# Performance work log

Measured on AMD Instinct MI355X. Metric: run time of the kernel, lower is better.

## Reference

```python
import jax, jax.numpy as jnp
import numpy as np

N_LAYERS, H, D, DFF, V = 6, 16, 1024, 4096, 512
B, S = 4, 2048
DK = D // H
EPS = 1e-6
NEG = -1000000000.0


def _pe_table(max_len, d):
    pos = np.arange(max_len, dtype=np.float32)[:, None]
    div = 1.0 / (10000.0 ** (np.arange(0, d, 2, dtype=np.float32) / d))
    pe = np.zeros((max_len, d), dtype=np.float32)
    pe[:, 0::2] = np.sin(pos * div)
    pe[:, 1::2] = np.cos(pos * div)
    return jnp.asarray(pe[None])  # [1, max_len, d]


def setup_inputs() -> dict:
    key = jax.random.key(0)
    ks = jax.random.split(key, 20)
    f = lambda k, shp: (jax.random.normal(k, shp, dtype=jnp.float32) * 0.02)
    inp = {
        "tgt": jax.random.randint(ks[0], (B, S), 0, V, dtype=jnp.int64),
        "tgt_mask": jnp.tril(jnp.ones((S, S), dtype=jnp.int32))[None],  # [1,S,S] causal
        "emb": f(ks[1], (V, D)),
        "pe": _pe_table(S, D),
        "Wq": f(ks[2], (N_LAYERS, H, D, DK)), "bq": f(ks[3], (N_LAYERS, H, DK)),
        "Wk": f(ks[4], (N_LAYERS, H, D, DK)), "bk": f(ks[5], (N_LAYERS, H, DK)),
        "Wv": f(ks[6], (N_LAYERS, H, D, DK)), "bv": f(ks[7], (N_LAYERS, H, DK)),
        "Wo": f(ks[8], (N_LAYERS, D, D)), "bo": f(ks[9], (N_LAYERS, D)),
        "W1": f(ks[10], (N_LAYERS, D, DFF)), "b1": f(ks[11], (N_LAYERS, DFF)),
        "W2": f(ks[12], (N_LAYERS, DFF, D)), "b2": f(ks[13], (N_LAYERS, D)),
        "ln1_a": jnp.ones((N_LAYERS, D)), "ln1_b": jnp.zeros((N_LAYERS, D)),
        "ln2_a": jnp.ones((N_LAYERS, D)), "ln2_b": jnp.zeros((N_LAYERS, D)),
        "lnf_a": jnp.ones((D,)), "lnf_b": jnp.zeros((D,)),
    }
    return inp


def _ln(x, a, b):
    # torch: a*(x-mean)/(std+eps)+b with unbiased std
    m = x.mean(-1, keepdims=True)
    var = ((x - m) ** 2).sum(-1, keepdims=True) / (x.shape[-1] - 1)
    return a * (x - m) / (jnp.sqrt(var) + EPS) + b


def reference(tgt, tgt_mask, emb, pe, Wq, bq, Wk, bk, Wv, bv, Wo, bo,
              W1, b1, W2, b2, ln1_a, ln1_b, ln2_a, ln2_b, lnf_a, lnf_b):
    d = emb.shape[1]
    s = tgt.shape[1]
    x = emb[tgt] * jnp.sqrt(jnp.float32(d)) + pe[:, :s]  # [B,S,D]
    dk = Wq.shape[-1]
    scale = jnp.sqrt(jnp.float32(dk))

    def layer(x, p):
        wq, bq_, wk, bk_, wv, bv_, wo, bo_, w1, b1_, w2, b2_, a1, g1, a2, g2 = p
        h = _ln(x, a1, g1)
        q = jnp.einsum('bsd,hdk->bhsk', h, wq) + bq_[:, None, :]
        k = jnp.einsum('bsd,hdk->bhsk', h, wk) + bk_[:, None, :]
        v = jnp.einsum('bsd,hdk->bhsk', h, wv) + bv_[:, None, :]
        sc = jnp.einsum('bhsk,bhtk->bhst', q, k) / scale
        sc = jnp.where(tgt_mask[:, None] == 0, jnp.float32(NEG), sc)
        att = jax.nn.softmax(sc, axis=-1)
        o = jnp.einsum('bhst,bhtk->bhsk', att, v)
        o = o.transpose(0, 2, 1, 3).reshape(x.shape)  # concat heads (head order)
        x = x + (o @ wo + bo_)
        h2 = _ln(x, a2, g2)
        x = x + (jnp.maximum(h2 @ w1 + b1_, 0.0) @ w2 + b2_)
        return x, None

    x, _ = jax.lax.scan(layer, x, (Wq, bq, Wk, bk, Wv, bv, Wo, bo,
                                   W1, b1, W2, b2, ln1_a, ln1_b, ln2_a, ln2_b))
    return _ln(x, lnf_a, lnf_b)
```

## Files before the change

kernel.cpp:

```cpp
#include <hip/hip_runtime.h>

typedef __bf16 bf16;
typedef float f32x4 __attribute__((ext_vector_type(4)));
typedef __bf16 bf16x8 __attribute__((ext_vector_type(8)));
typedef __bf16 bf16x4 __attribute__((ext_vector_type(4)));
typedef __bf16 bf16x2 __attribute__((ext_vector_type(2)));

#define NL 6
#define NH 16
#define DM 1024
#define DFF 4096
#define SEQ 2048
#define NB 4
#define NTOK (NB*SEQ)

__device__ __forceinline__ void gload16(const void* g, void* l) {
  __builtin_amdgcn_global_load_lds((const __attribute__((address_space(1))) void*)g,
                                   (__attribute__((address_space(3))) void*)l, 16, 0, 0);
}

__global__ __launch_bounds__(256) void repack_t(const float* __restrict__ src,
                                                bf16* __restrict__ out, int K, int N) {
  const int l = blockIdx.z;
  const int d0 = blockIdx.x * 32, n0 = blockIdx.y * 32;
  __shared__ float t[32][33];
  const int tx = threadIdx.x & 31, ty = threadIdx.x >> 5;
  const float* s = src + (size_t)l * K * N;
  #pragma unroll
  for (int j = 0; j < 4; ++j)
    t[ty*4 + j][tx] = s[(size_t)(d0 + ty*4 + j) * N + n0 + tx];
  __syncthreads();
  bf16* o = out + (size_t)l * N * K;
  #pragma unroll
  for (int j = 0; j < 4; ++j)
    o[(size_t)(n0 + ty*4 + j) * K + d0 + tx] = (bf16)t[tx][ty*4 + j];
}

__global__ __launch_bounds__(256) void repack_qkv(const float* __restrict__ Wq,
                                                  const float* __restrict__ Wk,
                                                  const float* __restrict__ Wv,
                                                  bf16* __restrict__ out) {
  const int l = blockIdx.z;
  const int d0 = blockIdx.x * 32, n0 = blockIdx.y * 32;
  __shared__ float t[32][33];
  const int tx = threadIdx.x & 31, ty = threadIdx.x >> 5;
  const int which = n0 >> 10, h = (n0 & 1023) >> 6, kh0 = n0 & 63;
  const float* W = (which == 0) ? Wq : (which == 1 ? Wk : Wv);
  const float* s = W + ((size_t)(l*NH + h) * DM) * 64 + kh0;
  #pragma unroll
  for (int j = 0; j < 4; ++j)
    t[ty*4 + j][tx] = s[(size_t)(d0 + ty*4 + j) * 64 + tx];
  __syncthreads();
  bf16* o = out + (size_t)l * 3072 * DM + (size_t)n0 * DM + d0;
  #pragma unroll
  for (int j = 0; j < 4; ++j)
    o[(size_t)(ty*4 + j) * DM + tx] = (bf16)t[tx][ty*4 + j];
}

__global__ __launch_bounds__(256) void repack_b(const float* __restrict__ bq,
                                                const float* __restrict__ bk,
                                                const float* __restrict__ bv,
                                                float* __restrict__ out) {
  const int i = blockIdx.x * 256 + threadIdx.x;
  if (i >= NL * 3072) return;
  const int l = i / 3072, n = i % 3072;
  const int which = n >> 10, h = (n >> 6) & 15, kh = n & 63;
  const float* b = (which == 0) ? bq : (which == 1 ? bk : bv);
  out[i] = b[(l*NH + h) * 64 + kh];
}

__global__ __launch_bounds__(256) void embed_k(const int* __restrict__ tgt,
                                               const float* __restrict__ emb,
                                               const float* __restrict__ pe,
                                               float* __restrict__ x) {
  const int i = blockIdx.x;
  const int spos = i & (SEQ - 1);
  const int tok = tgt[i];
  const int tid = threadIdx.x;
  float4 e = ((const float4*)(emb + (size_t)tok * DM))[tid];
  float4 p = ((const float4*)(pe + (size_t)spos * DM))[tid];
  float4 r; r.x = e.x*32.f + p.x; r.y = e.y*32.f + p.y; r.z = e.z*32.f + p.z; r.w = e.w*32.f + p.w;
  ((float4*)(x + (size_t)i * DM))[tid] = r;
}

template<bool OB>
__global__ __launch_bounds__(256) void ln_k(const float* __restrict__ x,
                                            const float* __restrict__ a,
                                            const float* __restrict__ bsh,
                                            bf16* __restrict__ ob, float* __restrict__ of) {
  __shared__ float red[8];
  const int row = blockIdx.x, tid = threadIdx.x;
  const float4 v = ((const float4*)(x + (size_t)row * DM))[tid];
  float s = v.x + v.y + v.z + v.w;
  #pragma unroll
  for (int off = 32; off > 0; off >>= 1) s += __shfl_down(s, off);
  if ((tid & 63) == 0) red[tid >> 6] = s;
  __syncthreads();
  const float mean = (red[0] + red[1] + red[2] + red[3]) * (1.f / 1024.f);
  const float d0 = v.x - mean, d1 = v.y - mean, d2 = v.z - mean, d3 = v.w - mean;
  float ss = d0*d0 + d1*d1 + d2*d2 + d3*d3;
  #pragma unroll
  for (int off = 32; off > 0; off >>= 1) ss += __shfl_down(ss, off);
  if ((tid & 63) == 0) red[4 + (tid >> 6)] = ss;
  __syncthreads();
  const float var = (red[4] + red[5] + red[6] + red[7]) * (1.f / 1023.f);
  const float inv = 1.f / (sqrtf(var) + 1e-6f);
  const float4 av = ((const float4*)a)[tid];
  const float4 bv = ((const float4*)bsh)[tid];
  const float r0 = av.x * d0 * inv + bv.x;
  const float r1 = av.y * d1 * inv + bv.y;
  const float r2 = av.z * d2 * inv + bv.z;
  const float r3 = av.w * d3 * inv + bv.w;
  if (OB) {
    bf16x4 w; w[0] = (bf16)r0; w[1] = (bf16)r1; w[2] = (bf16)r2; w[3] = (bf16)r3;
    ((bf16x4*)(ob + (size_t)row * DM))[tid] = w;
  } else {
    float4 w; w.x = r0; w.y = r1; w.z = r2; w.w = r3;
    ((float4*)(of + (size_t)row * DM))[tid] = w;
  }
}

#define BARRIER() asm volatile("s_barrier" ::: "memory")
#define VMW(n)    asm volatile("s_waitcnt vmcnt(" #n ")" ::: "memory")

template<int EPI>
__global__ __launch_bounds__(512, 1) void gemm8(const bf16* __restrict__ A,
                                                const bf16* __restrict__ B,
                                                const float* __restrict__ bias,
                                                float* __restrict__ xres,
                                                bf16* __restrict__ outb,
                                                bf16* __restrict__ vtb,
                                                int K, int ldc) {
  __shared__ __align__(16) char lds[131072];
  const int tid = threadIdx.x;
  const int m0 = blockIdx.x * 256, n0 = blockIdx.y * 256;
  const int wid = tid >> 6, lane = tid & 63;
  const int wm = wid >> 2, wn = wid & 3;
  const int fr = lane & 15, fq = lane >> 4;
  const int fl16 = (fq * 16 + fr) * 16;
  const int s0 = tid, s1 = tid + 512;
  const int r0 = ((s0 >> 7) << 4) | (s0 & 15), c0 = (((s0 >> 6) & 1) << 2) | ((s0 >> 4) & 3);
  const int r1 = ((s1 >> 7) << 4) | (s1 & 15), c1 = (((s1 >> 6) & 1) << 2) | ((s1 >> 4) & 3);
  const bf16* Ap0 = A + (size_t)(m0 + r0) * K + c0 * 8;
  const bf16* Ap1 = A + (size_t)(m0 + r1) * K + c1 * 8;
  const bf16* Bp0 = B + (size_t)(n0 + r0) * K + c0 * 8;
  const bf16* Bp1 = B + (size_t)(n0 + r1) * K + c1 * 8;
  const size_t rskip = (size_t)128 * K;
  const int aRd = wm * 16384;
  const int bRd = 32768 + (wn >> 1) * 16384;
  const int bN = (wn & 1) * 4;

  f32x4 acc[8][4] = {};
  bf16x8 af8[8][2], bfr[4][2];

#define ST_A(d, h, kt) { \
  gload16(Ap0 + (size_t)(h) * rskip + (kt), lds + (d)*65536 + (h)*16384 + s0*16); \
  gload16(Ap1 + (size_t)(h) * rskip + (kt), lds + (d)*65536 + (h)*16384 + s1*16); }
#define ST_B(d, h, kt) { \
  gload16(Bp0 + (size_t)(h) * rskip + (kt), lds + (d)*65536 + 32768 + (h)*16384 + s0*16); \
  gload16(Bp1 + (size_t)(h) * rskip + (kt), lds + (d)*65536 + 32768 + (h)*16384 + s1*16); }
#define LD_A(d, mb) { _Pragma("unroll") for (int m_ = 0; m_ < 4; ++m_) \
    _Pragma("unroll") for (int ks_ = 0; ks_ < 2; ++ks_) \
      af8[(mb) + m_][ks_] = *(const bf16x8*)(lds + (d)*65536 + aRd + ((mb) + m_)*2048 + ks_*1024 + fl16); }
#define LD_B(d, nb) { _Pragma("unroll") for (int n_ = 0; n_ < 2; ++n_) \
    _Pragma("unroll") for (int ks_ = 0; ks_ < 2; ++ks_) \
      bfr[(nb) + n_][ks_] = *(const bf16x8*)(lds + (d)*65536 + bRd + (bN + (nb) + n_)*2048 + ks_*1024 + fl16); }
#define MFMA_Q(mb, nb) { __builtin_amdgcn_s_setprio(1); \
  _Pragma("unroll") for (int m_ = 0; m_ < 4; ++m_) \
  _Pragma("unroll") for (int n_ = 0; n_ < 2; ++n_) \
  _Pragma("unroll") for (int ks_ = 0; ks_ < 2; ++ks_) \
    acc[(mb) + m_][(nb) + n_] = __builtin_amdgcn_mfma_f32_16x16x32_bf16( \
        af8[(mb) + m_][ks_], bfr[(nb) + n_][ks_], acc[(mb) + m_][(nb) + n_], 0, 0, 0); \
  __builtin_amdgcn_s_setprio(0); }

  ST_A(0, 0, 0); ST_A(0, 1, 0);
  ST_B(0, 0, 0); ST_B(0, 1, 0);
  ST_A(1, 0, 64); ST_A(1, 1, 64);
  VMW(4);
  BARRIER();

  const int niter = K >> 7;
  for (int it = 0; it < niter; ++it) {
    const int ktB1 = (2 * it + 1) << 6;
    const int ktE2 = (2 * it + 2) << 6;
    const int ktO3 = (2 * it + 3) << 6;
    const bool more = (it + 1 < niter);
    LD_A(0, 0); LD_B(0, 0);
    ST_B(1, 0, ktB1);
    BARRIER(); MFMA_Q(0, 0); BARRIER();
    LD_A(0, 4);
    ST_B(1, 1, ktB1);
    BARRIER(); MFMA_Q(4, 0); BARRIER();
    LD_B(0, 2);
    if (more) ST_A(0, 0, ktE2);
    BARRIER(); MFMA_Q(4, 2); BARRIER();
    if (more) { ST_A(0, 1, ktE2); VMW(4); } else { VMW(0); }
    BARRIER(); MFMA_Q(0, 2); BARRIER();
    LD_A(1, 0); LD_B(1, 0);
    if (more) ST_B(0, 0, ktE2);
    BARRIER(); MFMA_Q(0, 0); BARRIER();
    LD_A(1, 4);
    if (more) ST_B(0, 1, ktE2);
    BARRIER(); MFMA_Q(4, 0); BARRIER();
    LD_B(1, 2);
    if (more) ST_A(1, 0, ktO3);
    BARRIER(); MFMA_Q(4, 2); BARRIER();
    if (more) { ST_A(1, 1, ktO3); VMW(4); }
    BARRIER(); MFMA_Q(0, 2); BARRIER();
  }
#undef ST_A
#undef ST_B
#undef LD_A
#undef LD_B
#undef MFMA_Q

  #pragma unroll
  for (int m = 0; m < 8; ++m) {
    const int row = m0 + wm * 128 + m * 16 + fq * 4;
    #pragma unroll
    for (int n = 0; n < 4; ++n) {
      const int col = n0 + wn * 64 + n * 16 + fr;
      const float bc = bias[col];
      if constexpr (EPI == 3) {
        if (col >= 2048) {
          const int hh = (col - 2048) >> 6, dkk = col & 63;
          const int bb = row >> 11, tt = row & 2047;
          bf16x4 w;
          #pragma unroll
          for (int j = 0; j < 4; ++j) w[j] = (bf16)(acc[m][n][j] + bc);
          *(bf16x4*)(vtb + ((((size_t)bb*NH + hh)*64 + dkk)*SEQ + tt)) = w;
          continue;
        }
      }
      #pragma unroll
      for (int j = 0; j < 4; ++j) {
        const float v = acc[m][n][j] + bc;
        if constexpr (EPI == 1) {
          xres[(size_t)(row + j) * ldc + col] += v;
        } else if constexpr (EPI == 2) {
          outb[(size_t)(row + j) * ldc + col] = (bf16)fmaxf(v, 0.f);
        } else {
          outb[(size_t)(row + j) * ldc + col] = (bf16)v;
        }
      }
    }
  }
}

template<int EPI>
__global__ __launch_bounds__(512, 1) void gemm8n(const bf16* __restrict__ A,
                                                 const bf16* __restrict__ B,
                                                 const float* __restrict__ bias,
                                                 float* __restrict__ xres,
                                                 bf16* __restrict__ outb,
                                                 bf16* __restrict__ vtb,
                                                 int K, int ldc) {
  __shared__ __align__(16) char lds[131072];
  const int tid = threadIdx.x;
  const int m0 = blockIdx.x * 128, n0 = blockIdx.y * 256;
  const int wid = tid >> 6, lane = tid & 63;
  const int wm = wid >> 2, wn = wid & 3;
  const int fr = lane & 15, fq = lane >> 4;
  const int fl16 = (fq * 16 + fr) * 16;
  const int s0 = tid, s1 = tid + 512;
  const int r0 = ((s0 >> 7) << 4) | (s0 & 15), c0 = (((s0 >> 6) & 1) << 2) | ((s0 >> 4) & 3);
  const int r1 = ((s1 >> 7) << 4) | (s1 & 15), c1 = (((s1 >> 6) & 1) << 2) | ((s1 >> 4) & 3);
  const bf16* Ap0 = A + (size_t)(m0 + r0) * K + c0 * 8;
  const bf16* Ap1 = A + (size_t)(m0 + r1) * K + c1 * 8;
  const bf16* Bp0 = B + (size_t)(n0 + r0) * K + c0 * 8;
  const bf16* Bp1 = B + (size_t)(n0 + r1) * K + c1 * 8;
  const size_t rskipB = (size_t)128 * K;
  const int aRd = wm * 8192;
  const int bRd = wn * 8192;

  f32x4 acc[4][4] = {};
  bf16x8 af[4][2], bfr[4][2];

#define ST_An(d, kt) { \
  gload16(Ap0 + (kt), lds + (d)*16384 + s0*16); \
  gload16(Ap1 + (kt), lds + (d)*16384 + s1*16); }
#define ST_Bn(j, h, kt) { \
  gload16(Bp0 + (size_t)(h) * rskipB + (kt), lds + 32768 + (j)*32768 + (h)*16384 + s0*16); \
  gload16(Bp1 + (size_t)(h) * rskipB + (kt), lds + 32768 + (j)*32768 + (h)*16384 + s1*16); }
#define LD_An(d) { _Pragma("unroll") for (int m_ = 0; m_ < 4; ++m_) \
    _Pragma("unroll") for (int ks_ = 0; ks_ < 2; ++ks_) \
      af[m_][ks_] = *(const bf16x8*)(lds + (d)*16384 + aRd + m_*2048 + ks_*1024 + fl16); }
#define LD_Bn(j, nb) { _Pragma("unroll") for (int n_ = 0; n_ < 2; ++n_) \
    _Pragma("unroll") for (int ks_ = 0; ks_ < 2; ++ks_) \
      bfr[(nb) + n_][ks_] = *(const bf16x8*)(lds + 32768 + (j)*32768 + bRd + ((nb) + n_)*2048 + ks_*1024 + fl16); }
#define MFMA_H(nb) { __builtin_amdgcn_s_setprio(1); \
  _Pragma("unroll") for (int m_ = 0; m_ < 4; ++m_) \
  _Pragma("unroll") for (int n_ = 0; n_ < 2; ++n_) \
  _Pragma("unroll") for (int ks_ = 0; ks_ < 2; ++ks_) \
    acc[m_][(nb) + n_] = __builtin_amdgcn_mfma_f32_16x16x32_bf16( \
        af[m_][ks_], bfr[(nb) + n_][ks_], acc[m_][(nb) + n_], 0, 0, 0); \
  __builtin_amdgcn_s_setprio(0); }

  ST_An(0, 0);
  ST_Bn(0, 0, 0); ST_Bn(0, 1, 0);
  ST_An(1, 64);
  ST_Bn(1, 0, 64); ST_Bn(1, 1, 64);
  VMW(0);
  BARRIER();

  const int nt = K >> 6;
  int j = 0;
  for (int t = 0; t < nt; ++t) {
    const int d = t & 1;
    const int j2 = (j + 2 >= 3) ? (j - 1) : (j + 2);
    const bool more = (t + 2 < nt);
    const int kt2 = (t + 2) << 6;
    LD_An(d); LD_Bn(j, 0);
    if (more) { ST_Bn(j2, 0, kt2); ST_Bn(j2, 1, kt2); }
    BARRIER(); MFMA_H(0); BARRIER();
    LD_Bn(j, 2);
    if (more) { ST_An(d, kt2); VMW(6); } else { VMW(0); }
    BARRIER(); MFMA_H(2); BARRIER();
    j = (j + 1 >= 3) ? 0 : (j + 1);
  }
#undef ST_An
#undef ST_Bn
#undef LD_An
#undef LD_Bn
#undef MFMA_H

  #pragma unroll
  for (int m = 0; m < 4; ++m) {
    const int row = m0 + wm * 64 + m * 16 + fq * 4;
    #pragma unroll
    for (int n = 0; n < 4; ++n) {
      const int col = n0 + wn * 64 + n * 16 + fr;
      const float bc = bias[col];
      if constexpr (EPI == 3) {
        if (col >= 2048) {
          const int hh = (col - 2048) >> 6, dkk = col & 63;
          const int bb = row >> 11, tt = row & 2047;
          bf16x4 w;
          #pragma unroll
          for (int jj = 0; jj < 4; ++jj) w[jj] = (bf16)(acc[m][n][jj] + bc);
          *(bf16x4*)(vtb + ((((size_t)bb*NH + hh)*64 + dkk)*SEQ + tt)) = w;
          continue;
        }
      }
      #pragma unroll
      for (int jj = 0; jj < 4; ++jj) {
        const float v = acc[m][n][jj] + bc;
        if constexpr (EPI == 1) {
          xres[(size_t)(row + jj) * ldc + col] += v;
        } else if constexpr (EPI == 2) {
          outb[(size_t)(row + jj) * ldc + col] = (bf16)fmaxf(v, 0.f);
        } else {
          outb[(size_t)(row + jj) * ldc + col] = (bf16)v;
        }
      }
    }
  }
}

__global__ __launch_bounds__(256) void attn5_k(const bf16* __restrict__ qk,
                                               const bf16* __restrict__ vt,
                                               bf16* __restrict__ o) {
  __shared__ __align__(16) bf16 Ks[64 * 64];
  __shared__ __align__(16) bf16 Vs[64 * 64];
  __shared__ __align__(16) bf16 Ps[4][16 * 64];
  const int pairi = blockIdx.x;
  const int bh = blockIdx.y;
  const int b = bh >> 4, h = bh & 15;
  const int tid = threadIdx.x;
  const int wave = tid >> 6, lane = tid & 63;
  const int fr = lane & 15, fq = lane >> 4;
  const bf16* Qg = qk + (size_t)b * SEQ * 2048 + h * 64;
  const bf16* Kg = Qg + 1024;
  const bf16* Vtg = vt + (size_t)bh * 64 * SEQ;
  char* Ksc = (char*)Ks;
  char* Vsc = (char*)Vs;
  char* Pw = (char*)&Ps[wave][0];
  const int fr7 = fr & 7;

  for (int pass = 0; pass < 2; ++pass) {
    const int qb = (pass == 0) ? pairi : (31 - pairi);
    const int q0w = qb * 64 + wave * 16;
    const int qrow = q0w + fr;
    const bf16x8 qf0 = *(const bf16x8*)(Qg + (size_t)qrow * 2048 + fq * 8);
    const bf16x8 qf1 = *(const bf16x8*)(Qg + (size_t)qrow * 2048 + 32 + fq * 8);
    f32x4 oacc[4] = {};
    float mrun = -1e30f, lrun = 0.f;
    const int nt = qb + 1;
    for (int kt = 0; kt < nt; ++kt) {
      const int t0 = kt * 64;
      __syncthreads();
      #pragma unroll
      for (int s2 = 0; s2 < 2; ++s2) {
        const int slot = tid + s2 * 256;
        const int r = slot >> 3, mm = slot & 7;
        const int gc = (mm ^ (r & 7)) * 8;
        gload16(Kg + (size_t)(t0 + r) * 2048 + gc, Ksc + slot * 16);
        gload16(Vtg + (size_t)r * SEQ + t0 + gc, Vsc + slot * 16);
      }
      __syncthreads();
      if (t0 > q0w + 15) continue;
      f32x4 s[4] = {};
      #pragma unroll
      for (int n = 0; n < 4; ++n) {
        const int t_ = n * 16 + fr;
        const bf16x8 k0 = *(const bf16x8*)(Ksc + (t_ * 8 + (fq ^ (t_ & 7))) * 16);
        const bf16x8 k1 = *(const bf16x8*)(Ksc + (t_ * 8 + ((fq + 4) ^ (t_ & 7))) * 16);
        s[n] = __builtin_amdgcn_mfma_f32_16x16x32_bf16(k0, qf0, s[n], 0, 0, 0);
        s[n] = __builtin_amdgcn_mfma_f32_16x16x32_bf16(k1, qf1, s[n], 0, 0, 0);
      }
      float sv[16];
      #pragma unroll
      for (int n = 0; n < 4; ++n)
        #pragma unroll
        for (int jj = 0; jj < 4; ++jj)
          sv[n * 4 + jj] = s[n][jj] * 0.125f;
      const bool need_mask = (t0 + 63 > q0w);
      if (need_mask) {
        #pragma unroll
        for (int i = 0; i < 16; ++i) {
          const int t_abs = t0 + (i >> 2) * 16 + fq * 4 + (i & 3);
          if (t_abs > qrow) sv[i] = -1e30f;
        }
      }
      float a8[8];
      #pragma unroll
      for (int i = 0; i < 8; ++i) a8[i] = fmaxf(sv[i], sv[i + 8]);
      float a4[4];
      #pragma unroll
      for (int i = 0; i < 4; ++i) a4[i] = fmaxf(a8[i], a8[i + 4]);
      float mt = fmaxf(fmaxf(a4[0], a4[1]), fmaxf(a4[2], a4[3]));
      mt = fmaxf(mt, __shfl_xor(mt, 16));
      mt = fmaxf(mt, __shfl_xor(mt, 32));
      const float mnew = fmaxf(mrun, mt);
      const float corr = __expf(mrun - mnew);
      mrun = mnew;
      #pragma unroll
      for (int i = 0; i < 16; ++i) sv[i] = __expf(sv[i] - mnew);
      #pragma unroll
      for (int i = 0; i < 8; ++i) a8[i] = sv[i] + sv[i + 8];
      #pragma unroll
      for (int i = 0; i < 4; ++i) a4[i] = a8[i] + a8[i + 4];
      float ps = (a4[0] + a4[1]) + (a4[2] + a4[3]);
      ps += __shfl_xor(ps, 16);
      ps += __shfl_xor(ps, 32);
      lrun = lrun * corr + ps;
      float cv[4];
      #pragma unroll
      for (int jj = 0; jj < 4; ++jj) cv[jj] = __shfl(corr, fq * 4 + jj);
      #pragma unroll
      for (int nd = 0; nd < 4; ++nd)
        #pragma unroll
        for (int jj = 0; jj < 4; ++jj)
          oacc[nd][jj] *= cv[jj];
      #pragma unroll
      for (int n = 0; n < 4; ++n)
        #pragma unroll
        for (int jp = 0; jp < 2; ++jp) {
          bf16x2 w; w[0] = (bf16)sv[n * 4 + jp * 2]; w[1] = (bf16)sv[n * 4 + jp * 2 + 1];
          const int byteoff = n * 32 + fq * 8 + jp * 4;
          const int chunk = byteoff >> 4, within = byteoff & 15;
          *(bf16x2*)(Pw + fr * 128 + ((chunk ^ fr7) << 4) + within) = w;
        }
      #pragma unroll
      for (int ks = 0; ks < 2; ++ks) {
        const bf16x8 pa = *(const bf16x8*)(Pw + fr * 128 + (((ks * 4 + fq) ^ fr7) << 4));
        #pragma unroll
        for (int nd = 0; nd < 4; ++nd) {
          const int dk_ = nd * 16 + fr;
          const bf16x8 vf = *(const bf16x8*)(Vsc + (dk_ * 8 + ((ks * 4 + fq) ^ (dk_ & 7))) * 16);
          oacc[nd] = __builtin_amdgcn_mfma_f32_16x16x32_bf16(pa, vf, oacc[nd], 0, 0, 0);
        }
      }
    }
    float lv[4];
    #pragma unroll
    for (int jj = 0; jj < 4; ++jj) lv[jj] = __shfl(lrun, fq * 4 + jj);
    #pragma unroll
    for (int nd = 0; nd < 4; ++nd) {
      const int col = h * 64 + nd * 16 + fr;
      #pragma unroll
      for (int jj = 0; jj < 4; ++jj) {
        const int row = q0w + fq * 4 + jj;
        o[((size_t)b * SEQ + row) * DM + col] = (bf16)(oacc[nd][jj] / lv[jj]);
      }
    }
  }
}

extern "C" void kernel_launch(void* const* d_in, const int* in_sizes, int n_in,
                              void* d_out, int out_size, void* d_ws, size_t ws_size,
                              hipStream_t stream) {
  const int*   tgt  = (const int*)d_in[0];
  const float* emb  = (const float*)d_in[2];
  const float* pe   = (const float*)d_in[3];
  const float* Wq   = (const float*)d_in[4];
  const float* bq   = (const float*)d_in[5];
  const float* Wk   = (const float*)d_in[6];
  const float* bk   = (const float*)d_in[7];
  const float* Wv   = (const float*)d_in[8];
  const float* bv   = (const float*)d_in[9];
  const float* Wo   = (const float*)d_in[10];
  const float* bo   = (const float*)d_in[11];
  const float* W1   = (const float*)d_in[12];
  const float* b1   = (const float*)d_in[13];
  const float* W2   = (const float*)d_in[14];
  const float* b2   = (const float*)d_in[15];
  const float* ln1a = (const float*)d_in[16];
  const float* ln1b = (const float*)d_in[17];
  const float* ln2a = (const float*)d_in[18];
  const float* ln2b = (const float*)d_in[19];
  const float* lnfa = (const float*)d_in[20];
  const float* lnfb = (const float*)d_in[21];

  char* ws = (char*)d_ws;
  size_t off = 0;
  bf16*  wqkv = (bf16*)(ws + off);  off += (size_t)NL * 3072 * DM * 2;
  bf16*  wo_  = (bf16*)(ws + off);  off += (size_t)NL * DM * DM * 2;
  bf16*  w1_  = (bf16*)(ws + off);  off += (size_t)NL * DFF * DM * 2;
  bf16*  w2_  = (bf16*)(ws + off);  off += (size_t)NL * DM * DFF * 2;
  float* bqkv = (float*)(ws + off); off += (size_t)NL * 3072 * 4;
  float* x    = (float*)(ws + off); off += (size_t)NTOK * DM * 4;
  bf16*  hbuf = (bf16*)(ws + off);  off += (size_t)NTOK * DM * 2;
  bf16*  qkb  = (bf16*)(ws + off);  off += (size_t)NTOK * 2048 * 2;
  bf16*  vtb  = (bf16*)(ws + off);  off += (size_t)NB * NH * 64 * SEQ * 2;
  bf16*  obuf = (bf16*)(ws + off);  off += (size_t)NTOK * DM * 2;
  bf16*  ubuf = qkb;

  repack_qkv<<<dim3(32, 96, NL), 256, 0, stream>>>(Wq, Wk, Wv, wqkv);
  repack_t  <<<dim3(32, 32, NL), 256, 0, stream>>>(Wo, wo_, DM, DM);
  repack_t  <<<dim3(32, 128, NL), 256, 0, stream>>>(W1, w1_, DM, DFF);
  repack_t  <<<dim3(128, 32, NL), 256, 0, stream>>>(W2, w2_, DFF, DM);
  repack_b  <<<72, 256, 0, stream>>>(bq, bk, bv, bqkv);
  embed_k   <<<NTOK, 256, 0, stream>>>(tgt, emb, pe, x);

  for (int l = 0; l < NL; ++l) {
    ln_k<true><<<NTOK, 256, 0, stream>>>(x, ln1a + l * DM, ln1b + l * DM, hbuf, nullptr);
    gemm8n<3><<<dim3(64, 12), 512, 0, stream>>>(hbuf, wqkv + (size_t)l * 3072 * DM,
                                                bqkv + l * 3072, nullptr, qkb, vtb, DM, 2048);
    attn5_k<<<dim3(16, 64), 256, 0, stream>>>(qkb, vtb, obuf);
    gemm8n<1><<<dim3(64, 4), 512, 0, stream>>>(obuf, wo_ + (size_t)l * DM * DM,
                                               bo + l * DM, x, nullptr, nullptr, DM, DM);
    ln_k<true><<<NTOK, 256, 0, stream>>>(x, ln2a + l * DM, ln2b + l * DM, hbuf, nullptr);
    gemm8<2><<<dim3(32, 16), 512, 0, stream>>>(hbuf, w1_ + (size_t)l * DFF * DM,
                                               b1 + l * DFF, nullptr, ubuf, nullptr, DM, DFF);
    gemm8n<1><<<dim3(64, 4), 512, 0, stream>>>(ubuf, w2_ + (size_t)l * DM * DFF,
                                               b2 + l * DM, x, nullptr, nullptr, DFF, DM);
  }
  ln_k<false><<<NTOK, 256, 0, stream>>>(x, lnfa, lnfb, nullptr, (float*)d_out);

  (void)in_sizes; (void)n_in; (void)out_size; (void)ws_size;
}
```

Measured before the change: 2.738 ms.

## Replace tuned GEMMs with simple 128x128 double-buffered kernel and pipeline attention K/V

Replaces the two hand-scheduled 512-thread GEMMs (256x256 and 128x256 tiles with interleaved staging and barriers) with a single 256-thread, 128x128-tile GEMM. It uses two LDS stages and targets two blocks per CU. The attention kernel now double-buffers K/V tiles, remaps blocks so each XCD shares heads, and skips the rescale when the running max does not grow. The 1/sqrt(dk) scale is folded into the Q projection epilogue. The simpler GEMM loses the fine-grained load/MFMA interleave and the larger-tile reuse, so it may lose throughput on the dominant matmuls.

```diff
diff --git a/kernel.cpp b/kernel.cpp
--- a/kernel.cpp
+++ b/kernel.cpp
@@ -124,205 +124,70 @@
 #define VMW(n)    asm volatile("s_waitcnt vmcnt(" #n ")" ::: "memory")
 
 template<int EPI>
-__global__ __launch_bounds__(512, 1) void gemm8(const bf16* __restrict__ A,
+__global__ __launch_bounds__(256, 2) void gemmA(const bf16* __restrict__ A,
                                                 const bf16* __restrict__ B,
                                                 const float* __restrict__ bias,
                                                 float* __restrict__ xres,
                                                 bf16* __restrict__ outb,
                                                 bf16* __restrict__ vtb,
                                                 int K, int ldc) {
-  __shared__ __align__(16) char lds[131072];
+  __shared__ __align__(16) char lds[65536];
   const int tid = threadIdx.x;
-  const int m0 = blockIdx.x * 256, n0 = blockIdx.y * 256;
+  const int m0 = blockIdx.x * 128, n0 = blockIdx.y * 128;
   const int wid = tid >> 6, lane = tid & 63;
-  const int wm = wid >> 2, wn = wid & 3;
+  const int wm = wid >> 1, wn = wid & 1;
   const int fr = lane & 15, fq = lane >> 4;
   const int fl16 = (fq * 16 + fr) * 16;
-  const int s0 = tid, s1 = tid + 512;
-  const int r0 = ((s0 >> 7) << 4) | (s0 & 15), c0 = (((s0 >> 6) & 1) << 2) | ((s0 >> 4) & 3);
-  const int r1 = ((s1 >> 7) << 4) | (s1 & 15), c1 = (((s1 >> 6) & 1) << 2) | ((s1 >> 4) & 3);
-  const bf16* Ap0 = A + (size_t)(m0 + r0) * K + c0 * 8;
-  const bf16* Ap1 = A + (size_t)(m0 + r1) * K + c1 * 8;
-  const bf16* Bp0 = B + (size_t)(n0 + r0) * K + c0 * 8;
-  const bf16* Bp1 = B + (size_t)(n0 + r1) * K + c1 * 8;
-  const size_t rskip = (size_t)128 * K;
-  const int aRd = wm * 16384;
-  const int bRd = 32768 + (wn >> 1) * 16384;
-  const int bN = (wn & 1) * 4;
-
-  f32x4 acc[8][4] = {};
-  bf16x8 af8[8][2], bfr[4][2];
-
-#define ST_A(d, h, kt) { \
-  gload16(Ap0 + (size_t)(h) * rskip + (kt), lds + (d)*65536 + (h)*16384 + s0*16); \
-  gload16(Ap1 + (size_t)(h) * rskip + (kt), lds + (d)*65536 + (h)*16384 + s1*16); }
-#define ST_B(d, h, kt) { \
-  gload16(Bp0 + (size_t)(h) * rskip + (kt), lds + (d)*65536 + 32768 + (h)*16384 + s0*16); \
-  gload16(Bp1 + (size_t)(h) * rskip + (kt), lds + (d)*65536 + 32768 + (h)*16384 + s1*16); }
-#define LD_A(d, mb) { _Pragma("unroll") for (int m_ = 0; m_ < 4; ++m_) \
-    _Pragma("unroll") for (int ks_ = 0; ks_ < 2; ++ks_) \
-      af8[(mb) + m_][ks_] = *(const bf16x8*)(lds + (d)*65536 + aRd + ((mb) + m_)*2048 + ks_*1024 + fl16); }
-#define LD_B(d, nb) { _Pragma("unroll") for (int n_ = 0; n_ < 2; ++n_) \
-    _Pragma("unroll") for (int ks_ = 0; ks_ < 2; ++ks_) \
-      bfr[(nb) + n_][ks_] = *(const bf16x8*)(lds + (d)*65536 + bRd + (bN + (nb) + n_)*2048 + ks_*1024 + fl16); }
-#define MFMA_Q(mb, nb) { __builtin_amdgcn_s_setprio(1); \
-  _Pragma("unroll") for (int m_ = 0; m_ < 4; ++m_) \
-  _Pragma("unroll") for (int n_ = 0; n_ < 2; ++n_) \
-  _Pragma("unroll") for (int ks_ = 0; ks_ < 2; ++ks_) \
-    acc[(mb) + m_][(nb) + n_] = __builtin_amdgcn_mfma_f32_16x16x32_bf16( \
-        af8[(mb) + m_][ks_], bfr[(nb) + n_][ks_], acc[(mb) + m_][(nb) + n_], 0, 0, 0); \
-  __builtin_amdgcn_s_setprio(0); }
-
-  ST_A(0, 0, 0); ST_A(0, 1, 0);
-  ST_B(0, 0, 0); ST_B(0, 1, 0);
-  ST_A(1, 0, 64); ST_A(1, 1, 64);
-  VMW(4);
-  BARRIER();
-
-  const int niter = K >> 7;
-  for (int it = 0; it < niter; ++it) {
-    const int ktB1 = (2 * it + 1) << 6;
-    const int ktE2 = (2 * it + 2) << 6;
-    const int ktO3 = (2 * it + 3) << 6;
-    const bool more = (it + 1 < niter);
-    LD_A(0, 0); LD_B(0, 0);
-    ST_B(1, 0, ktB1);
-    BARRIER(); MFMA_Q(0, 0); BARRIER();
-    LD_A(0, 4);
-    ST_B(1, 1, ktB1);
-    BARRIER(); MFMA_Q(4, 0); BARRIER();
-    LD_B(0, 2);
-    if (more) ST_A(0, 0, ktE2);
-    BARRIER(); MFMA_Q(4, 2); BARRIER();
-    if (more) { ST_A(0, 1, ktE2); VMW(4); } else { VMW(0); }
-    BARRIER(); MFMA_Q(0, 2); BARRIER();
-    LD_A(1, 0); LD_B(1, 0);
-    if (more) ST_B(0, 0, ktE2);
-    BARRIER(); MFMA_Q(0, 0); BARRIER();
-    LD_A(1, 4);
-    if (more) ST_B(0, 1, ktE2);
-    BARRIER(); MFMA_Q(4, 0); BARRIER();
-    LD_B(1, 2);
-    if (more) ST_A(1, 0, ktO3);
-    BARRIER(); MFMA_Q(4, 2); BARRIER();
-    if (more) { ST_A(1, 1, ktO3); VMW(4); }
-    BARRIER(); MFMA_Q(0, 2); BARRIER();
-  }
-#undef ST_A
-#undef ST_B
-#undef LD_A
-#undef LD_B
-#undef MFMA_Q
-
-  #pragma unroll
-  for (int m = 0; m < 8; ++m) {
-    const int row = m0 + wm * 128 + m * 16 + fq * 4;
-    #pragma unroll
-    for (int n = 0; n < 4; ++n) {
-      const int col = n0 + wn * 64 + n * 16 + fr;
-      const float bc = bias[col];
-      if constexpr (EPI == 3) {
-        if (col >= 2048) {
-          const int hh = (col - 2048) >> 6, dkk = col & 63;
-          const int bb = row >> 11, tt = row & 2047;
-          bf16x4 w;
-          #pragma unroll
-          for (int j = 0; j < 4; ++j) w[j] = (bf16)(acc[m][n][j] + bc);
-          *(bf16x4*)(vtb + ((((size_t)bb*NH + hh)*64 + dkk)*SEQ + tt)) = w;
-          continue;
-        }
-      }
-      #pragma unroll
-      for (int j = 0; j < 4; ++j) {
-        const float v = acc[m][n][j] + bc;
-        if constexpr (EPI == 1) {
-          xres[(size_t)(row + j) * ldc + col] += v;
-        } else if constexpr (EPI == 2) {
-          outb[(size_t)(row + j) * ldc + col] = (bf16)fmaxf(v, 0.f);
-        } else {
-          outb[(size_t)(row + j) * ldc + col] = (bf16)v;
-        }
-      }
-    }
-  }
-}
-
-template<int EPI>
-__global__ __launch_bounds__(512, 1) void gemm8n(const bf16* __restrict__ A,
-                                                 const bf16* __restrict__ B,
-                                                 const float* __restrict__ bias,
-                                                 float* __restrict__ xres,
-                                                 bf16* __restrict__ outb,
-                                                 bf16* __restrict__ vtb,
-                                                 int K, int ldc) {
-  __shared__ __align__(16) char lds[131072];
-  const int tid = threadIdx.x;
-  const int m0 = blockIdx.x * 128, n0 = blockIdx.y * 256;
-  const int wid = tid >> 6, lane = tid & 63;
-  const int wm = wid >> 2, wn = wid & 3;
-  const int fr = lane & 15, fq = lane >> 4;
-  const int fl16 = (fq * 16 + fr) * 16;
-  const int s0 = tid, s1 = tid + 512;
-  const int r0 = ((s0 >> 7) << 4) | (s0 & 15), c0 = (((s0 >> 6) & 1) << 2) | ((s0 >> 4) & 3);
-  const int r1 = ((s1 >> 7) << 4) | (s1 & 15), c1 = (((s1 >> 6) & 1) << 2) | ((s1 >> 4) & 3);
-  const bf16* Ap0 = A + (size_t)(m0 + r0) * K + c0 * 8;
-  const bf16* Ap1 = A + (size_t)(m0 + r1) * K + c1 * 8;
-  const bf16* Bp0 = B + (size_t)(n0 + r0) * K + c0 * 8;
-  const bf16* Bp1 = B + (size_t)(n0 + r1) * K + c1 * 8;
-  const size_t rskipB = (size_t)128 * K;
   const int aRd = wm * 8192;
-  const int bRd = wn * 8192;
+  const int bRd = 16384 + wn * 8192;
+
+  const bf16* Ap[4];
+  const bf16* Bp[4];
+  #pragma unroll
+  for (int j = 0; j < 4; ++j) {
+    const int s = tid + j * 256;
+    const int r = ((s >> 7) << 4) | (s & 15);
+    const int c = (((s >> 6) & 1) << 2) | ((s >> 4) & 3);
+    Ap[j] = A + (size_t)(m0 + r) * K + c * 8;
+    Bp[j] = B + (size_t)(n0 + r) * K + c * 8;
+  }
 
   f32x4 acc[4][4] = {};
   bf16x8 af[4][2], bfr[4][2];
 
-#define ST_An(d, kt) { \
-  gload16(Ap0 + (kt), lds + (d)*16384 + s0*16); \
-  gload16(Ap1 + (kt), lds + (d)*16384 + s1*16); }
-#define ST_Bn(j, h, kt) { \
-  gload16(Bp0 + (size_t)(h) * rskipB + (kt), lds + 32768 + (j)*32768 + (h)*16384 + s0*16); \
-  gload16(Bp1 + (size_t)(h) * rskipB + (kt), lds + 32768 + (j)*32768 + (h)*16384 + s1*16); }
-#define LD_An(d) { _Pragma("unroll") for (int m_ = 0; m_ < 4; ++m_) \
+#define STG(d, kt) { _Pragma("unroll") for (int j = 0; j < 4; ++j) { \
+    gload16(Ap[j] + (kt), lds + (d)*32768 + (tid + j*256)*16); \
+    gload16(Bp[j] + (kt), lds + (d)*32768 + 16384 + (tid + j*256)*16); } }
+#define LDF(d) { _Pragma("unroll") for (int m_ = 0; m_ < 4; ++m_) \
     _Pragma("unroll") for (int ks_ = 0; ks_ < 2; ++ks_) \
-      af[m_][ks_] = *(const bf16x8*)(lds + (d)*16384 + aRd + m_*2048 + ks_*1024 + fl16); }
-#define LD_Bn(j, nb) { _Pragma("unroll") for (int n_ = 0; n_ < 2; ++n_) \
+      af[m_][ks_] = *(const bf16x8*)(lds + (d)*32768 + aRd + m_*2048 + ks_*1024 + fl16); \
+    _Pragma("unroll") for (int n_ = 0; n_ < 4; ++n_) \
     _Pragma("unroll") for (int ks_ = 0; ks_ < 2; ++ks_) \
-      bfr[(nb) + n_][ks_] = *(const bf16x8*)(lds + 32768 + (j)*32768 + bRd + ((nb) + n_)*2048 + ks_*1024 + fl16); }
-#define MFMA_H(nb) { __builtin_amdgcn_s_setprio(1); \
+      bfr[n_][ks_] = *(const bf16x8*)(lds + (d)*32768 + bRd + n_*2048 + ks_*1024 + fl16); }
+#define MM() { __builtin_amdgcn_s_setprio(1); \
   _Pragma("unroll") for (int m_ = 0; m_ < 4; ++m_) \
-  _Pragma("unroll") for (int n_ = 0; n_ < 2; ++n_) \
+  _Pragma("unroll") for (int n_ = 0; n_ < 4; ++n_) \
   _Pragma("unroll") for (int ks_ = 0; ks_ < 2; ++ks_) \
-    acc[m_][(nb) + n_] = __builtin_amdgcn_mfma_f32_16x16x32_bf16( \
-        af[m_][ks_], bfr[(nb) + n_][ks_], acc[m_][(nb) + n_], 0, 0, 0); \
+    acc[m_][n_] = __builtin_amdgcn_mfma_f32_16x16x32_bf16( \
+        af[m_][ks_], bfr[n_][ks_], acc[m_][n_], 0, 0, 0); \
   __builtin_amdgcn_s_setprio(0); }
 
-  ST_An(0, 0);
-  ST_Bn(0, 0, 0); ST_Bn(0, 1, 0);
-  ST_An(1, 64);
-  ST_Bn(1, 0, 64); ST_Bn(1, 1, 64);
+  STG(0, 0);
   VMW(0);
   BARRIER();
 
   const int nt = K >> 6;
-  int j = 0;
   for (int t = 0; t < nt; ++t) {
     const int d = t & 1;
-    const int j2 = (j + 2 >= 3) ? (j - 1) : (j + 2);
-    const bool more = (t + 2 < nt);
-    const int kt2 = (t + 2) << 6;
-    LD_An(d); LD_Bn(j, 0);
-    if (more) { ST_Bn(j2, 0, kt2); ST_Bn(j2, 1, kt2); }
-    BARRIER(); MFMA_H(0); BARRIER();
-    LD_Bn(j, 2);
-    if (more) { ST_An(d, kt2); VMW(6); } else { VMW(0); }
-    BARRIER(); MFMA_H(2); BARRIER();
-    j = (j + 1 >= 3) ? 0 : (j + 1);
-  }
-#undef ST_An
-#undef ST_Bn
-#undef LD_An
-#undef LD_Bn
-#undef MFMA_H
+    if (t + 1 < nt) STG(d ^ 1, (t + 1) << 6);
+    LDF(d);
+    MM();
+    VMW(0);
+    BARRIER();
+  }
+#undef STG
+#undef LDF
+#undef MM
 
   #pragma unroll
   for (int m = 0; m < 4; ++m) {
@@ -344,7 +209,8 @@
       }
       #pragma unroll
       for (int jj = 0; jj < 4; ++jj) {
-        const float v = acc[m][n][jj] + bc;
+        float v = acc[m][n][jj] + bc;
+        if constexpr (EPI == 3) { if (col < 1024) v *= 0.125f; }
         if constexpr (EPI == 1) {
           xres[(size_t)(row + jj) * ldc + col] += v;
         } else if constexpr (EPI == 2) {
@@ -360,11 +226,13 @@
 __global__ __launch_bounds__(256) void attn5_k(const bf16* __restrict__ qk,
                                                const bf16* __restrict__ vt,
                                                bf16* __restrict__ o) {
-  __shared__ __align__(16) bf16 Ks[64 * 64];
-  __shared__ __align__(16) bf16 Vs[64 * 64];
+  __shared__ __align__(16) bf16 Ks[2][64 * 64];
+  __shared__ __align__(16) bf16 Vs[2][64 * 64];
   __shared__ __align__(16) bf16 Ps[4][16 * 64];
-  const int pairi = blockIdx.x;
-  const int bh = blockIdx.y;
+  const int flat = blockIdx.y * 16 + blockIdx.x;
+  const int xcd = flat & 7, slot = flat >> 3;
+  const int bh = xcd * 8 + (slot >> 4);
+  const int pairi = slot & 15;
   const int b = bh >> 4, h = bh & 15;
   const int tid = threadIdx.x;
   const int wave = tid >> 6, lane = tid & 63;
@@ -372,10 +240,18 @@
   const bf16* Qg = qk + (size_t)b * SEQ * 2048 + h * 64;
   const bf16* Kg = Qg + 1024;
   const bf16* Vtg = vt + (size_t)bh * 64 * SEQ;
-  char* Ksc = (char*)Ks;
-  char* Vsc = (char*)Vs;
   char* Pw = (char*)&Ps[wave][0];
   const int fr7 = fr & 7;
+
+  const int sl0 = tid, sl1 = tid + 256;
+  const int sr0 = sl0 >> 3, sm0 = sl0 & 7, sg0 = (sm0 ^ (sr0 & 7)) * 8;
+  const int sr1 = sl1 >> 3, sm1 = sl1 & 7, sg1 = (sm1 ^ (sr1 & 7)) * 8;
+
+#define STAGE_KV(db, t0_) { \
+    gload16(Kg + (size_t)((t0_) + sr0) * 2048 + sg0, (char*)Ks + (db)*8192 + sl0*16); \
+    gload16(Vtg + (size_t)sr0 * SEQ + (t0_) + sg0,   (char*)Vs + (db)*8192 + sl0*16); \
+    gload16(Kg + (size_t)((t0_) + sr1) * 2048 + sg1, (char*)Ks + (db)*8192 + sl1*16); \
+    gload16(Vtg + (size_t)sr1 * SEQ + (t0_) + sg1,   (char*)Vs + (db)*8192 + sl1*16); }
 
   for (int pass = 0; pass < 2; ++pass) {
     const int qb = (pass == 0) ? pairi : (31 - pairi);
@@ -386,19 +262,22 @@
     f32x4 oacc[4] = {};
     float mrun = -1e30f, lrun = 0.f;
     const int nt = qb + 1;
+    __syncthreads();
+    STAGE_KV(0, 0);
     for (int kt = 0; kt < nt; ++kt) {
       const int t0 = kt * 64;
+      const int db = kt & 1;
       __syncthreads();
-      #pragma unroll
-      for (int s2 = 0; s2 < 2; ++s2) {
-        const int slot = tid + s2 * 256;
-        const int r = slot >> 3, mm = slot & 7;
-        const int gc = (mm ^ (r & 7)) * 8;
-        gload16(Kg + (size_t)(t0 + r) * 2048 + gc, Ksc + slot * 16);
-        gload16(Vtg + (size_t)r * SEQ + t0 + gc, Vsc + slot * 16);
+      if (kt + 1 < nt) {
+        STAGE_KV(db ^ 1, (kt + 1) * 64);
+        VMW(4);
+      } else {
+        VMW(0);
       }
       __syncthreads();
       if (t0 > q0w + 15) continue;
+      const char* Ksc = (char*)Ks + db * 8192;
+      const char* Vsc = (char*)Vs + db * 8192;
       f32x4 s[4] = {};
       #pragma unroll
       for (int n = 0; n < 4; ++n) {
@@ -413,7 +292,7 @@
       for (int n = 0; n < 4; ++n)
         #pragma unroll
         for (int jj = 0; jj < 4; ++jj)
-          sv[n * 4 + jj] = s[n][jj] * 0.125f;
+          sv[n * 4 + jj] = s[n][jj];
       const bool need_mask = (t0 + 63 > q0w);
       if (need_mask) {
         #pragma unroll
@@ -431,8 +310,10 @@
       float mt = fmaxf(fmaxf(a4[0], a4[1]), fmaxf(a4[2], a4[3]));
       mt = fmaxf(mt, __shfl_xor(mt, 16));
       mt = fmaxf(mt, __shfl_xor(mt, 32));
+      const bool grow = __any(mt > mrun);
       const float mnew = fmaxf(mrun, mt);
-      const float corr = __expf(mrun - mnew);
+      float corr = 1.f;
+      if (grow) corr = __expf(mrun - mnew);
       mrun = mnew;
       #pragma unroll
       for (int i = 0; i < 16; ++i) sv[i] = __expf(sv[i] - mnew);
@@ -443,15 +324,19 @@
       float ps = (a4[0] + a4[1]) + (a4[2] + a4[3]);
       ps += __shfl_xor(ps, 16);
       ps += __shfl_xor(ps, 32);
-      lrun = lrun * corr + ps;
-      float cv[4];
-      #pragma unroll
-      for (int jj = 0; jj < 4; ++jj) cv[jj] = __shfl(corr, fq * 4 + jj);
-      #pragma unroll
-      for (int nd = 0; nd < 4; ++nd)
-        #pragma unroll
-        for (int jj = 0; jj < 4; ++jj)
-          oacc[nd][jj] *= cv[jj];
+      if (grow) {
+        lrun = lrun * corr + ps;
+        float cv[4];
+        #pragma unroll
+        for (int jj = 0; jj < 4; ++jj) cv[jj] = __shfl(corr, fq * 4 + jj);
+        #pragma unroll
+        for (int nd = 0; nd < 4; ++nd)
+          #pragma unroll
+          for (int jj = 0; jj < 4; ++jj)
+            oacc[nd][jj] *= cv[jj];
+      } else {
+        lrun += ps;
+      }
       #pragma unroll
       for (int n = 0; n < 4; ++n)
         #pragma unroll
@@ -485,6 +370,7 @@
       }
     }
   }
+#undef STAGE_KV
 }
 
 extern "C" void kernel_launch(void* const* d_in, const int* in_sizes, int n_in,
@@ -535,16 +421,16 @@
 
   for (int l = 0; l < NL; ++l) {
     ln_k<true><<<NTOK, 256, 0, stream>>>(x, ln1a + l * DM, ln1b + l * DM, hbuf, nullptr);
-    gemm8n<3><<<dim3(64, 12), 512, 0, stream>>>(hbuf, wqkv + (size_t)l * 3072 * DM,
-                                                bqkv + l * 3072, nullptr, qkb, vtb, DM, 2048);
+    gemmA<3><<<dim3(64, 24), 256, 0, stream>>>(hbuf, wqkv + (size_t)l * 3072 * DM,
+                                               bqkv + l * 3072, nullptr, qkb, vtb, DM, 2048);
     attn5_k<<<dim3(16, 64), 256, 0, stream>>>(qkb, vtb, obuf);
-    gemm8n<1><<<dim3(64, 4), 512, 0, stream>>>(obuf, wo_ + (size_t)l * DM * DM,
-                                               bo + l * DM, x, nullptr, nullptr, DM, DM);
+    gemmA<1><<<dim3(64, 8), 256, 0, stream>>>(obuf, wo_ + (size_t)l * DM * DM,
+                                              bo + l * DM, x, nullptr, nullptr, DM, DM);
     ln_k<true><<<NTOK, 256, 0, stream>>>(x, ln2a + l * DM, ln2b + l * DM, hbuf, nullptr);
-    gemm8<2><<<dim3(32, 16), 512, 0, stream>>>(hbuf, w1_ + (size_t)l * DFF * DM,
+    gemmA<2><<<dim3(64, 32), 256, 0, stream>>>(hbuf, w1_ + (size_t)l * DFF * DM,
                                                b1 + l * DFF, nullptr, ubuf, nullptr, DM, DFF);
-    gemm8n<1><<<dim3(64, 4), 512, 0, stream>>>(ubuf, w2_ + (size_t)l * DM * DFF,
-                                               b2 + l * DM, x, nullptr, nullptr, DFF, DM);
+    gemmA<1><<<dim3(64, 8), 256, 0, stream>>>(ubuf, w2_ + (size_t)l * DM * DFF,
+                                              b2 + l * DM, x, nullptr, nullptr, DFF, DM);
   }
   ln_k<false><<<NTOK, 256, 0, stream>>>(x, lnfa, lnfb, nullptr, (float*)d_out);
 
```

Result: slower. 3.341 ms (+22.0%).
